# Performance work log

Hardware: AMD Instinct MI355X
Metric: run time of the kernel (lower is better)

## Reference

```python
import jax, jax.numpy as jnp
import numpy as np

B = 32
H = W = 64
C = 128
HEADS = 4
HEAD_DIM = C // HEADS
WS = 8            # window_size
SS = 4            # shift_size
N = WS * WS       # tokens per window
MLP_HID = 4 * C
SCALE = HEAD_DIM ** -0.5
EPS = 1e-5


def _rel_pos_index():
    coords = np.stack(np.meshgrid(np.arange(WS), np.arange(WS), indexing='ij'))
    cf = coords.reshape(2, -1)
    rel = (cf[:, :, None] - cf[:, None, :]).transpose(1, 2, 0)
    rel[:, :, 0] += WS - 1
    rel[:, :, 1] += WS - 1
    rel[:, :, 0] *= 2 * WS - 1
    return rel.sum(-1)  # (N, N) int


def _attn_mask():
    img_mask = np.zeros((1, H, W, 1), np.float32)
    slices = (slice(0, -WS), slice(-WS, -SS), slice(-SS, None))
    cnt = 0
    for hs in slices:
        for ws in slices:
            img_mask[:, hs, ws, :] = cnt
            cnt += 1
    mw = img_mask.reshape(1, H // WS, WS, W // WS, WS, 1)
    mw = mw.transpose(0, 1, 3, 2, 4, 5).reshape(-1, N)  # (nW, N)
    am = mw[:, None, :] - mw[:, :, None]
    return np.where(am != 0, np.float32(-100.0), np.float32(0.0))  # (nW, N, N)


REL_POS_IDX = jnp.asarray(_rel_pos_index().reshape(-1))  # (N*N,)
ATTN_MASK = jnp.asarray(_attn_mask())                    # (nW, N, N)


def setup_inputs() -> dict:
    key = jax.random.key(0)
    ks = jax.random.split(key, 12)
    s = 0.02
    return {
        'x': jax.random.normal(ks[0], (B, H * W, C), jnp.float32),
        'norm1_g': jnp.ones((C,), jnp.float32),
        'norm1_b': jnp.zeros((C,), jnp.float32),
        'qkv_w': jax.random.normal(ks[1], (C, 3 * C), jnp.float32) * s,
        'qkv_b': jnp.zeros((3 * C,), jnp.float32),
        'proj_w': jax.random.normal(ks[2], (C, C), jnp.float32) * s,
        'proj_b': jnp.zeros((C,), jnp.float32),
        'rpb_table': jax.random.normal(ks[3], ((2 * WS - 1) * (2 * WS - 1), HEADS), jnp.float32) * s,
        'norm2_g': jnp.ones((C,), jnp.float32),
        'norm2_b': jnp.zeros((C,), jnp.float32),
        'mlp_w1': jax.random.normal(ks[4], (C, MLP_HID), jnp.float32) * s,
        'mlp_b1': jnp.zeros((MLP_HID,), jnp.float32),
        'mlp_w2': jax.random.normal(ks[5], (MLP_HID, C), jnp.float32) * s,
        'mlp_b2': jnp.zeros((C,), jnp.float32),
    }


def _layernorm(x, g, b):
    m = x.mean(-1, keepdims=True)
    v = jnp.mean((x - m) ** 2, -1, keepdims=True)
    return (x - m) * jax.lax.rsqrt(v + EPS) * g + b


def reference(x, norm1_g, norm1_b, qkv_w, qkv_b, proj_w, proj_b, rpb_table,
              norm2_g, norm2_b, mlp_w1, mlp_b1, mlp_w2, mlp_b2):
    shortcut = x
    h = _layernorm(x, norm1_g, norm1_b).reshape(-1, H, W, C)
    # cyclic shift
    h = jnp.roll(h, (-SS, -SS), axis=(1, 2))
    # window partition -> (B*nW, N, C)
    hw = h.reshape(-1, H // WS, WS, W // WS, WS, C)
    hw = hw.transpose(0, 1, 3, 2, 4, 5).reshape(-1, N, C)
    # window attention
    qkv = (hw @ qkv_w + qkv_b).reshape(-1, N, 3, HEADS, HEAD_DIM)
    qkv = qkv.transpose(2, 0, 3, 1, 4)  # (3, B*nW, heads, N, hd)
    q, k, v = qkv[0] * SCALE, qkv[1], qkv[2]
    attn = jnp.einsum('bhnd,bhmd->bhnm', q, k)  # (B*nW, heads, N, N)
    rpb = rpb_table[REL_POS_IDX].reshape(N, N, HEADS).transpose(2, 0, 1)
    attn = attn + rpb[None]
    nW = ATTN_MASK.shape[0]
    attn = attn.reshape(-1, nW, HEADS, N, N) + ATTN_MASK[None, :, None]
    attn = jax.nn.softmax(attn.reshape(-1, HEADS, N, N), axis=-1)
    out = jnp.einsum('bhnm,bhmd->bhnd', attn, v)
    out = out.transpose(0, 2, 1, 3).reshape(-1, N, C)
    out = out @ proj_w + proj_b
    # window reverse
    out = out.reshape(-1, H // WS, W // WS, WS, WS, C)
    out = out.transpose(0, 1, 3, 2, 4, 5).reshape(-1, H, W, C)
    # reverse cyclic shift
    out = jnp.roll(out, (SS, SS), axis=(1, 2)).reshape(-1, H * W, C)
    x = shortcut + out
    # MLP branch
    h2 = _layernorm(x, norm2_g, norm2_b)
    h2 = jax.nn.gelu(h2 @ mlp_w1 + mlp_b1, approximate=False)
    h2 = h2 @ mlp_w2 + mlp_b2
    return x + h2
```

## Files before the change

### kernel.cpp

```cpp
#include <hip/hip_runtime.h>
#include <math.h>

typedef __attribute__((ext_vector_type(8))) short bf16x8;
typedef __attribute__((ext_vector_type(4))) short bf16x4;
typedef __attribute__((ext_vector_type(4))) float f32x4;
typedef __attribute__((ext_vector_type(4))) unsigned short u16x4;

#define DEVI __device__ __forceinline__

DEVI float b2f(unsigned int u){ union{unsigned int i; float f;} c; c.i = u<<16; return c.f; }
DEVI unsigned short f2b(float f){
  union{float f; unsigned int i;} c; c.f = f;
  unsigned int r = c.i + 0x7fffu + ((c.i>>16)&1u);
  return (unsigned short)(r>>16);
}
DEVI unsigned int pack2(float a, float b){
  return (unsigned int)f2b(a) | ((unsigned int)f2b(b)<<16);
}
DEVI void unpack8(uint4 u, float* f){
  f[0]=b2f(u.x&0xffffu); f[1]=b2f(u.x>>16);
  f[2]=b2f(u.y&0xffffu); f[3]=b2f(u.y>>16);
  f[4]=b2f(u.z&0xffffu); f[5]=b2f(u.z>>16);
  f[6]=b2f(u.w&0xffffu); f[7]=b2f(u.w>>16);
}
DEVI f32x4 mfma16(bf16x8 a, bf16x8 b, f32x4 c){
  return __builtin_amdgcn_mfma_f32_16x16x32_bf16(a, b, c, 0, 0, 0);
}
DEVI f32x4 mfma16x16(bf16x4 a, bf16x4 b, f32x4 c){
#if __has_builtin(__builtin_amdgcn_mfma_f32_16x16x16bf16_1k)
  return __builtin_amdgcn_mfma_f32_16x16x16bf16_1k(a, b, c, 0, 0, 0);
#else
  f32x4 d = c;
  asm volatile("v_mfma_f32_16x16x16_bf16 %0, %1, %2, %0" : "+v"(d) : "v"(a), "v"(b));
  return d;
#endif
}
DEVI float gelu_fast(float u){
  const float y2 = 1.5957691216057308f*(u + 0.044715f*u*u*u);
  return u / (1.f + __expf(-y2));
}
DEVI int swzA(int row, int byi){ return row*256 + (byi ^ ((row&7)<<4)); }
DEVI int swzQ(int row, int byi){ return row*64  + (byi ^ (((row>>1)&3)<<4)); }
DEVI int swzO(int row, int byc){ return row*512 + (byc ^ ((row&7)<<4) ^ (((byc>>7)&3)<<5)); }

__global__ void k_prep(const float* __restrict__ qkvw, const float* __restrict__ projw,
                       const float* __restrict__ w1,   const float* __restrict__ w2,
                       const float* __restrict__ rpbt,
                       ushort* __restrict__ qkvF, ushort* __restrict__ projF,
                       ushort* __restrict__ w1F,  ushort* __restrict__ w2F,
                       ushort* __restrict__ rpbE)
{
  const int t = blockIdx.x*256 + threadIdx.x;
  const int l = t&63, fr = t>>6;
  const int l15 = l&15, l4 = l>>4;
  {
    const int head = t>>12, q = (t>>6)&63, k = t&63;
    const int di = (q>>3)-(k>>3)+7, dj = (q&7)-(k&7)+7;
    rpbE[t] = f2b(rpbt[(di*15+dj)*4 + head]);
  }
  {
    const int c = fr>>5, og = (fr>>2)&7, h = fr&3;
    const int oc = og*16 + l15, hid0 = c*64 + h*16 + l4*4;
    ushort* d = w2F + (size_t)fr*256 + l*4;
    #pragma unroll
    for(int e=0;e<4;e++) d[e] = f2b(w2[(size_t)(hid0+e)*128 + oc]);
  }
  if (fr < 128){
    const int c = fr>>4, hg = (fr>>2)&3, kk = fr&3;
    const int hid = c*64 + hg*16 + l15, k0 = kk*32 + l4*8;
    ushort* d = w1F + (size_t)fr*512 + l*8;
    #pragma unroll
    for(int e=0;e<8;e++) d[e] = f2b(w1[(size_t)(k0+e)*512 + hid]);
  }
  if (fr < 96){
    const int s3 = fr>>5, g = (fr>>2)&7, kk = fr&3;
    const int col = s3*128 + g*16 + l15, k0 = kk*32 + l4*8;
    ushort* d = qkvF + (size_t)fr*512 + l*8;
    #pragma unroll
    for(int e=0;e<8;e++) d[e] = f2b(qkvw[(size_t)(k0+e)*384 + col]);
  }
  if (fr < 32){
    const int g = fr>>2, kk = fr&3;
    const int col = g*16 + l15, k0 = kk*32 + l4*8;
    ushort* d = projF + (size_t)fr*512 + l*8;
    #pragma unroll
    for(int e=0;e<8;e++) d[e] = f2b(projw[(size_t)(k0+e)*128 + col]);
  }
}

__global__ __launch_bounds__(256,3) void k_attn(
    const float*  __restrict__ x,
    const float*  __restrict__ g1, const float* __restrict__ be1,
    const ushort* __restrict__ qkvF, const float* __restrict__ qkvb,
    const ushort* __restrict__ projF, const float* __restrict__ projb,
    const ushort* __restrict__ rpbE,
    ushort* __restrict__ x2w)
{
  __shared__ __align__(16) char smem[49152];
  const int tid  = threadIdx.x;
  const int wave = tid>>6, lane = tid&63;
  const int l15 = lane&15, l4 = lane>>4;
  const int wid = blockIdx.x;
  const int b   = wid>>6, wim = wid&63;
  const int wh  = wim>>3, wv = wim&7;

  char* const smA  = smem;
  char* const smQ  = smem + 16384 + wave*8192;
  char* const smK  = smQ + 4096;
  char* const smR  = smem + 16384;

  const f32x4 Z = {0.f,0.f,0.f,0.f};
  const int t_row = tid>>2;
  const int cg    = (tid&3)*32;
  const int ti_r = t_row>>3, tj_r = t_row&7;
  const int ho_r = (wh*8+ti_r+4)&63, wo_r = (wv*8+tj_r+4)&63;
  const size_t growbase = ((size_t)(b*4096 + ho_r*64 + wo_r))*128;

  {
    const float* src = x + growbase + cg;
    float v[32];
    #pragma unroll
    for(int q=0;q<8;q++){
      const float4 f4 = *(const float4*)(src + q*4);
      v[q*4+0]=f4.x; v[q*4+1]=f4.y; v[q*4+2]=f4.z; v[q*4+3]=f4.w;
    }
    float s=0.f, ss=0.f;
    #pragma unroll
    for(int e=0;e<32;e++){ s+=v[e]; ss+=v[e]*v[e]; }
    s += __shfl_xor(s,1); ss += __shfl_xor(ss,1);
    s += __shfl_xor(s,2); ss += __shfl_xor(ss,2);
    const float mean = s*(1.f/128.f);
    const float varv = fmaxf(ss*(1.f/128.f) - mean*mean, 0.f);
    const float rstd = rsqrtf(varv + 1e-5f);
    #pragma unroll
    for(int q=0;q<4;q++){
      const float4 ga = *(const float4*)(g1 +cg+q*8);
      const float4 gb = *(const float4*)(g1 +cg+q*8+4);
      const float4 ba = *(const float4*)(be1+cg+q*8);
      const float4 bb = *(const float4*)(be1+cg+q*8+4);
      const float* vp = v + q*8;
      uint4 pk;
      pk.x = pack2((vp[0]-mean)*rstd*ga.x+ba.x, (vp[1]-mean)*rstd*ga.y+ba.y);
      pk.y = pack2((vp[2]-mean)*rstd*ga.z+ba.z, (vp[3]-mean)*rstd*ga.w+ba.w);
      pk.z = pack2((vp[4]-mean)*rstd*gb.x+bb.x, (vp[5]-mean)*rstd*gb.y+bb.y);
      pk.w = pack2((vp[6]-mean)*rstd*gb.z+bb.z, (vp[7]-mean)*rstd*gb.w+bb.w);
      *(uint4*)(smA + swzA(t_row, cg*2 + q*16)) = pk;
    }
  }
  __syncthreads();

  const int headc = wave*32;
  bf16x4 Vf[4][2];

  {
    #pragma unroll
    for(int s3=0;s3<3;s3++){
      f32x4 acc[4][2];
      #pragma unroll
      for(int rt=0;rt<4;rt++){ acc[rt][0]=Z; acc[rt][1]=Z; }
      bf16x8 bfr[2][4];
      #pragma unroll
      for(int ct=0;ct<2;ct++)
        #pragma unroll
        for(int kk=0;kk<4;kk++)
          bfr[ct][kk] = *(const bf16x8*)(qkvF + (size_t)((s3*8 + wave*2 + ct)*4 + kk)*512 + lane*8);
      #pragma unroll
      for(int kk=0;kk<4;kk++){
        bf16x8 afr[4];
        #pragma unroll
        for(int rt=0;rt<4;rt++)
          afr[rt] = *(const bf16x8*)(smA + swzA(rt*16+l15, kk*64 + l4*16));
        #pragma unroll
        for(int rt=0;rt<4;rt++)
          #pragma unroll
          for(int ct=0;ct<2;ct++)
            acc[rt][ct] = mfma16(afr[rt], bfr[ct][kk], acc[rt][ct]);
      }
      #pragma unroll
      for(int ct=0;ct<2;ct++){
        const int hd = ct*16 + l15;
        const float bias = qkvb[s3*128 + headc + hd];
        if (s3==2){
          #pragma unroll
          for(int rt=0;rt<4;rt++){
            union { uint2 u; bf16x4 v; } cv;
            cv.u.x = pack2(acc[rt][ct][0]+bias, acc[rt][ct][1]+bias);
            cv.u.y = pack2(acc[rt][ct][2]+bias, acc[rt][ct][3]+bias);
            Vf[rt][ct] = cv.v;
          }
        } else {
          char* const dst = (s3==0) ? smQ : smK;
          const float sc = (s3==0) ? 0.17677669529663687f : 1.f;
          #pragma unroll
          for(int rt=0;rt<4;rt++){
            const int t0 = rt*16 + l4*4;
            #pragma unroll
            for(int j=0;j<4;j++)
              *(ushort*)(dst + swzQ(t0+j, hd*2)) = f2b((acc[rt][ct][j]+bias)*sc);
          }
        }
      }
    }
  }
  __syncthreads();

  f32x4 O[4][2];
  #pragma unroll
  for(int rt=0;rt<4;rt++){ O[rt][0]=Z; O[rt][1]=Z; }
  {
    bf16x8 kfr[4];
    #pragma unroll
    for(int g=0; g<4; ++g)
      kfr[g] = *(const bf16x8*)(smK + swzQ(g*16+l15, l4*16));
    const bool edge = (wh==7) || (wv==7);
    #pragma unroll
    for(int rt=0; rt<4; ++rt){
      const bf16x8 qf = *(const bf16x8*)(smQ + swzQ(rt*16+l15, l4*16));
      f32x4 S[4];
      #pragma unroll
      for(int g=0; g<4; ++g)
        S[g] = mfma16(kfr[g], qf, Z);
      const int q = rt*16 + l15;
      int regq = 0;
      if (edge){
        const int qi=q>>3, qj=q&7;
        regq = ((wh<7)?0:((qi<4)?1:2))*3 + ((wv<7)?0:((qj<4)?1:2));
      }
      const ushort* rbase = rpbE + wave*4096 + q*64 + l4*4;
      #pragma unroll
      for(int g=0; g<4; ++g){
        const u16x4 rb = *(const u16x4*)(rbase + g*16);
        #pragma unroll
        for(int j=0;j<4;j++){
          float add = b2f(rb[j]);
          if (edge){
            const int k = g*16 + l4*4 + j;
            const int ki=k>>3, kj=k&7;
            const int regk = ((wh<7)?0:((ki<4)?1:2))*3 + ((wv<7)?0:((kj<4)?1:2));
            if (regk != regq) add -= 100.f;
          }
          S[g][j] += add;
        }
      }
      float mx = -1e30f;
      #pragma unroll
      for(int g=0;g<4;g++)
        #pragma unroll
        for(int j=0;j<4;j++) mx = fmaxf(mx, S[g][j]);
      mx = fmaxf(mx, __shfl_xor(mx,16));
      mx = fmaxf(mx, __shfl_xor(mx,32));
      float sm = 0.f;
      #pragma unroll
      for(int g=0;g<4;g++)
        #pragma unroll
        for(int j=0;j<4;j++){ const float e = __expf(S[g][j]-mx); S[g][j]=e; sm+=e; }
      sm += __shfl_xor(sm,16);
      sm += __shfl_xor(sm,32);
      const float inv = 1.f/sm;
      #pragma unroll
      for(int g=0;g<4;g++){
        union { uint2 u; bf16x4 v; } cv;
        cv.u.x = pack2(S[g][0]*inv, S[g][1]*inv);
        cv.u.y = pack2(S[g][2]*inv, S[g][3]*inv);
        #pragma unroll
        for(int cvi=0;cvi<2;cvi++)
          O[rt][cvi] = mfma16x16(cv.v, Vf[g][cvi], O[rt][cvi]);
      }
    }
    #pragma unroll
    for(int rt=0;rt<4;rt++)
      #pragma unroll
      for(int cvi=0;cvi<2;cvi++)
        #pragma unroll
        for(int j=0;j<4;j++)
          *(ushort*)(smA + swzA(rt*16+l4*4+j, (headc + cvi*16 + l15)*2)) = f2b(O[rt][cvi][j]);
  }
  __syncthreads();

  {
    f32x4 PR[4][2];
    #pragma unroll
    for(int rt=0;rt<4;rt++){ PR[rt][0]=Z; PR[rt][1]=Z; }
    bf16x8 pb[2][4];
    #pragma unroll
    for(int ct=0;ct<2;ct++)
      #pragma unroll
      for(int kk=0;kk<4;kk++)
        pb[ct][kk] = *(const bf16x8*)(projF + (size_t)((wave*2+ct)*4 + kk)*512 + lane*8);
    #pragma unroll
    for(int kk=0;kk<4;kk++){
      bf16x8 afr[4];
      #pragma unroll
      for(int rt=0;rt<4;rt++)
        afr[rt] = *(const bf16x8*)(smA + swzA(rt*16+l15, kk*64 + l4*16));
      #pragma unroll
      for(int rt=0;rt<4;rt++)
        #pragma unroll
        for(int ct=0;ct<2;ct++)
          PR[rt][ct] = mfma16(afr[rt], pb[ct][kk], PR[rt][ct]);
    }
    #pragma unroll
    for(int ct=0;ct<2;ct++){
      const int col = headc + ct*16 + l15;
      const float bias = projb[col];
      #pragma unroll
      for(int rt=0;rt<4;rt++)
        #pragma unroll
        for(int j=0;j<4;j++)
          *(float*)(smR + swzO(rt*16+l4*4+j, col*4)) = PR[rt][ct][j] + bias;
    }
  }
  __syncthreads();

  {
    const float* xsrc = x + growbase + cg;
    ushort* drow = x2w + ((size_t)(wid*64 + t_row))*128 + cg;
    #pragma unroll
    for(int q=0;q<4;q++){
      const f32x4 oa = *(const f32x4*)(smR + swzO(t_row, (cg+q*8  )*4));
      const f32x4 ob = *(const f32x4*)(smR + swzO(t_row, (cg+q*8+4)*4));
      const float4 xa = *(const float4*)(xsrc + q*8);
      const float4 xb = *(const float4*)(xsrc + q*8+4);
      uint4 pk;
      pk.x = pack2(oa[0]+xa.x, oa[1]+xa.y);
      pk.y = pack2(oa[2]+xa.z, oa[3]+xa.w);
      pk.z = pack2(ob[0]+xb.x, ob[1]+xb.y);
      pk.w = pack2(ob[2]+xb.z, ob[3]+xb.w);
      *(uint4*)(drow + q*8) = pk;
    }
  }
}

__global__ __launch_bounds__(1024) void k_mlp2(
    const ushort* __restrict__ x2w,
    const float* __restrict__ g2, const float* __restrict__ be2,
    const ushort* __restrict__ w1F, const float* __restrict__ bb1,
    const ushort* __restrict__ w2F, const float* __restrict__ bb2,
    float* __restrict__ outp)
{
  __shared__ __align__(16) char smem[65536];
  __shared__ float smB1[512];
  const int tid  = threadIdx.x;
  const int wave = tid>>6, lane = tid&63;
  const int l15 = lane&15, l4 = lane>>4;
  const int gblk = blockIdx.x;
  const f32x4 Z = {0.f,0.f,0.f,0.f};

  if (tid < 512) smB1[tid] = bb1[tid];

  {
    const int tk = tid>>2;
    const int cg = (tid&3)*32;
    const ushort* src = x2w + ((size_t)(gblk*256 + tk))*128 + cg;
    float v[32];
    unpack8(*(const uint4*)(src   ), v   );
    unpack8(*(const uint4*)(src+ 8), v+ 8);
    unpack8(*(const uint4*)(src+16), v+16);
    unpack8(*(const uint4*)(src+24), v+24);
    float s=0.f, ss=0.f;
    #pragma unroll
    for(int e=0;e<32;e++){ s+=v[e]; ss+=v[e]*v[e]; }
    s += __shfl_xor(s,1); ss += __shfl_xor(ss,1);
    s += __shfl_xor(s,2); ss += __shfl_xor(ss,2);
    const float mean = s*(1.f/128.f);
    const float varv = fmaxf(ss*(1.f/128.f) - mean*mean, 0.f);
    const float rstd = rsqrtf(varv + 1e-5f);
    #pragma unroll
    for(int q=0;q<4;q++){
      const float4 ga = *(const float4*)(g2 +cg+q*8);
      const float4 gb = *(const float4*)(g2 +cg+q*8+4);
      const float4 ba = *(const float4*)(be2+cg+q*8);
      const float4 bb = *(const float4*)(be2+cg+q*8+4);
      const float* vp = v + q*8;
      uint4 pk;
      pk.x = pack2((vp[0]-mean)*rstd*ga.x+ba.x, (vp[1]-mean)*rstd*ga.y+ba.y);
      pk.y = pack2((vp[2]-mean)*rstd*ga.z+ba.z, (vp[3]-mean)*rstd*ga.w+ba.w);
      pk.z = pack2((vp[4]-mean)*rstd*gb.x+bb.x, (vp[5]-mean)*rstd*gb.y+bb.y);
      pk.w = pack2((vp[6]-mean)*rstd*gb.z+bb.z, (vp[7]-mean)*rstd*gb.w+bb.w);
      *(uint4*)(smem + swzA(tk, cg*2 + q*16)) = pk;
    }
  }
  __syncthreads();

  const int trow = wave*16 + l15;
  bf16x8 xf[4];
  #pragma unroll
  for(int kk=0;kk<4;++kk)
    xf[kk] = *(const bf16x8*)(smem + swzA(trow, kk*64 + l4*16));
  __syncthreads();

  const ushort* const wsrc = (wave<8) ? w1F : w2F;
  const int ldsoff = ((wave<8)?0:16384) + (wave&7)*2048;
  const int subsh  = (wave&7)*1024;
  #define STAGE_CHUNK(cc, bufbase) do{ \
    const ushort* gsrc = wsrc + (size_t)(cc)*8192 + subsh + lane*8; \
    char* lb = (bufbase) + ldsoff; \
    __builtin_amdgcn_global_load_lds((const unsigned int*)(gsrc     ), (unsigned int*)(lb      ), 16, 0, 0); \
    __builtin_amdgcn_global_load_lds((const unsigned int*)(gsrc+512 ), (unsigned int*)(lb+1024 ), 16, 0, 0); \
  }while(0)

  STAGE_CHUNK(0, smem);
  STAGE_CHUNK(1, smem + 32768);

  f32x4 OA[8];
  #pragma unroll
  for(int ocg=0;ocg<8;++ocg) OA[ocg]=Z;

  for (int c=0; c<8; ++c){
    if (c < 7) asm volatile("s_waitcnt vmcnt(2)" ::: "memory");
    else       asm volatile("s_waitcnt vmcnt(0)" ::: "memory");
    __builtin_amdgcn_s_barrier();
    __builtin_amdgcn_sched_barrier(0);

    char* const buf = (c&1) ? (smem + 32768) : smem;
    const int hidb = c*64;
    f32x4 acc1[4] = {Z,Z,Z,Z};
    #pragma unroll
    for(int hg=0; hg<4; ++hg)
      #pragma unroll
      for(int kk=0; kk<4; ++kk){
        const bf16x8 wf = *(const bf16x8*)(buf + (hg*4+kk)*1024 + lane*16);
        acc1[hg] = mfma16(wf, xf[kk], acc1[hg]);
      }
    bf16x4 Hf[4];
    #pragma unroll
    for(int hg=0; hg<4; ++hg){
      const float4 b4 = *(const float4*)(&smB1[hidb + hg*16 + l4*4]);
      bf16x4 hv;
      hv[0] = (short)f2b(gelu_fast(acc1[hg][0]+b4.x));
      hv[1] = (short)f2b(gelu_fast(acc1[hg][1]+b4.y));
      hv[2] = (short)f2b(gelu_fast(acc1[hg][2]+b4.z));
      hv[3] = (short)f2b(gelu_fast(acc1[hg][3]+b4.w));
      Hf[hg] = hv;
    }
    #pragma unroll
    for(int ocg=0; ocg<8; ++ocg)
      #pragma unroll
      for(int hg=0; hg<4; ++hg){
        const bf16x4 w2f = *(const bf16x4*)(buf + 16384 + (ocg*4+hg)*512 + lane*8);
        OA[ocg] = mfma16x16(w2f, Hf[hg], OA[ocg]);
      }

    __builtin_amdgcn_sched_barrier(0);
    __builtin_amdgcn_s_barrier();
    __builtin_amdgcn_sched_barrier(0);
    if (c < 6) STAGE_CHUNK(c+2, (c&1) ? (smem + 32768) : smem);
  }
  #undef STAGE_CHUNK

  __syncthreads();
  {
    const int tk = tid>>2;
    const int cg = (tid&3)*32;
    const uint4* src = (const uint4*)(x2w + ((size_t)(gblk*256 + tk))*128 + cg);
    #pragma unroll
    for(int q=0;q<4;q++) *(uint4*)(smem + swzA(tk, cg*2 + q*16)) = src[q];
  }
  __syncthreads();
  {
    const int tk  = trow;
    const int wid = gblk*4 + (tk>>6);
    const int n   = tk & 63;
    const int bb  = wid>>6, wim = wid&63;
    const int wh  = wim>>3, wv = wim&7;
    const int ti  = n>>3,  tj = n&7;
    const int ho  = (wh*8+ti+4)&63, wo = (wv*8+tj+4)&63;
    float* const drow = outp + ((size_t)(bb*4096 + ho*64 + wo))*128;
    #pragma unroll
    for(int ocg=0; ocg<8; ++ocg){
      const int oc = ocg*16 + l4*4;
      const float4 b4 = *(const float4*)(bb2 + oc);
      const u16x4 xr = *(const u16x4*)(smem + swzA(tk, oc*2));
      f32x4 r = OA[ocg];
      r[0] += b4.x + b2f(xr[0]);
      r[1] += b4.y + b2f(xr[1]);
      r[2] += b4.z + b2f(xr[2]);
      r[3] += b4.w + b2f(xr[3]);
      __builtin_nontemporal_store(r, (f32x4*)(drow + oc));
    }
  }
}

extern "C" void kernel_launch(void* const* d_in, const int* in_sizes, int n_in,
                              void* d_out, int out_size, void* d_ws, size_t ws_size,
                              hipStream_t stream) {
  (void)in_sizes; (void)n_in; (void)out_size; (void)ws_size;
  const float* x     = (const float*)d_in[0];
  const float* n1g   = (const float*)d_in[1];
  const float* n1b   = (const float*)d_in[2];
  const float* qkvw  = (const float*)d_in[3];
  const float* qkvb  = (const float*)d_in[4];
  const float* projw = (const float*)d_in[5];
  const float* projb = (const float*)d_in[6];
  const float* rpbt  = (const float*)d_in[7];
  const float* n2g   = (const float*)d_in[8];
  const float* n2b   = (const float*)d_in[9];
  const float* w1    = (const float*)d_in[10];
  const float* b1    = (const float*)d_in[11];
  const float* w2    = (const float*)d_in[12];
  const float* b2    = (const float*)d_in[13];
  float* outp = (float*)d_out;

  ushort* ws    = (ushort*)d_ws;
  ushort* x2w   = ws;
  ushort* qkvF  = ws + 16777216;
  ushort* projF = qkvF + 49152;
  ushort* w1F   = projF + 16384;
  ushort* w2F   = w1F + 65536;
  ushort* rpbE  = w2F + 65536;

  k_prep<<<64, 256, 0, stream>>>(qkvw, projw, w1, w2, rpbt, qkvF, projF, w1F, w2F, rpbE);
  k_attn<<<2048, 256, 0, stream>>>(x, n1g, n1b, qkvF, qkvb, projF, projb, rpbE, x2w);
  k_mlp2<<<512, 1024, 0, stream>>>(x2w, n2g, n2b, w1F, b1, w2F, b2, outp);
}
```

Measured before the change: 185.7 us.

## Use hardware bf16 converts, pack W2 fragments, stage MLP output through LDS for coalesced stores

Replaces the software round-to-nearest bf16 packing with the HIP bf16 intrinsics, which may lower to packed convert instructions on this hardware. Reorders the prepared W2 layout so each lane loads 8 bf16 values per LDS read and feeds two 16x16x16 MFMAs, halving the W2 LDS loads. The final MLP output is rounded to bf16 and written to LDS, then re-read row-contiguously so each thread adds residual and bias and writes 32 contiguous floats per row instead of scattered 16-byte pieces. The trade is that the MLP output is now rounded to bf16 before the residual add, which loses precision, and an extra LDS round trip plus barrier is added.

```diff
diff --git a/kernel.cpp b/kernel.cpp
--- a/kernel.cpp
+++ b/kernel.cpp
@@ -1,4 +1,5 @@
 #include <hip/hip_runtime.h>
+#include <hip/hip_bf16.h>
 #include <math.h>
 
 typedef __attribute__((ext_vector_type(8))) short bf16x8;
@@ -14,8 +15,16 @@
   unsigned int r = c.i + 0x7fffu + ((c.i>>16)&1u);
   return (unsigned short)(r>>16);
 }
-DEVI unsigned int pack2(float a, float b){
-  return (unsigned int)f2b(a) | ((unsigned int)f2b(b)<<16);
+DEVI unsigned int cvtpk2(float a, float b){
+  union { __hip_bfloat162 h; unsigned int u; } c;
+  c.h.x = __float2bfloat16(a);
+  c.h.y = __float2bfloat16(b);
+  return c.u;
+}
+DEVI unsigned short f2b1(float a){
+  union { __hip_bfloat16 h; unsigned short u; } c;
+  c.h = __float2bfloat16(a);
+  return c.u;
 }
 DEVI void unpack8(uint4 u, float* f){
   f[0]=b2f(u.x&0xffffu); f[1]=b2f(u.x>>16);
@@ -58,12 +67,16 @@
     const int di = (q>>3)-(k>>3)+7, dj = (q&7)-(k&7)+7;
     rpbE[t] = f2b(rpbt[(di*15+dj)*4 + head]);
   }
-  {
-    const int c = fr>>5, og = (fr>>2)&7, h = fr&3;
-    const int oc = og*16 + l15, hid0 = c*64 + h*16 + l4*4;
-    ushort* d = w2F + (size_t)fr*256 + l*4;
-    #pragma unroll
-    for(int e=0;e<4;e++) d[e] = f2b(w2[(size_t)(hid0+e)*128 + oc]);
+  if (fr < 128){
+    const int c = fr>>4, ocg = (fr>>1)&7, hgp = fr&1;
+    const int oc = ocg*16 + l15;
+    const int hidA = c*64 + (hgp*2)*16 + l4*4;
+    ushort* d = w2F + (size_t)c*8192 + (ocg*2+hgp)*512 + l*8;
+    #pragma unroll
+    for(int e=0;e<4;e++){
+      d[e]   = f2b(w2[(size_t)(hidA+e   )*128 + oc]);
+      d[4+e] = f2b(w2[(size_t)(hidA+16+e)*128 + oc]);
+    }
   }
   if (fr < 128){
     const int c = fr>>4, hg = (fr>>2)&3, kk = fr&3;
@@ -140,10 +153,10 @@
       const float4 bb = *(const float4*)(be1+cg+q*8+4);
       const float* vp = v + q*8;
       uint4 pk;
-      pk.x = pack2((vp[0]-mean)*rstd*ga.x+ba.x, (vp[1]-mean)*rstd*ga.y+ba.y);
-      pk.y = pack2((vp[2]-mean)*rstd*ga.z+ba.z, (vp[3]-mean)*rstd*ga.w+ba.w);
-      pk.z = pack2((vp[4]-mean)*rstd*gb.x+bb.x, (vp[5]-mean)*rstd*gb.y+bb.y);
-      pk.w = pack2((vp[6]-mean)*rstd*gb.z+bb.z, (vp[7]-mean)*rstd*gb.w+bb.w);
+      pk.x = cvtpk2((vp[0]-mean)*rstd*ga.x+ba.x, (vp[1]-mean)*rstd*ga.y+ba.y);
+      pk.y = cvtpk2((vp[2]-mean)*rstd*ga.z+ba.z, (vp[3]-mean)*rstd*ga.w+ba.w);
+      pk.z = cvtpk2((vp[4]-mean)*rstd*gb.x+bb.x, (vp[5]-mean)*rstd*gb.y+bb.y);
+      pk.w = cvtpk2((vp[6]-mean)*rstd*gb.z+bb.z, (vp[7]-mean)*rstd*gb.w+bb.w);
       *(uint4*)(smA + swzA(t_row, cg*2 + q*16)) = pk;
     }
   }
@@ -184,8 +197,8 @@
           #pragma unroll
           for(int rt=0;rt<4;rt++){
             union { uint2 u; bf16x4 v; } cv;
-            cv.u.x = pack2(acc[rt][ct][0]+bias, acc[rt][ct][1]+bias);
-            cv.u.y = pack2(acc[rt][ct][2]+bias, acc[rt][ct][3]+bias);
+            cv.u.x = cvtpk2(acc[rt][ct][0]+bias, acc[rt][ct][1]+bias);
+            cv.u.y = cvtpk2(acc[rt][ct][2]+bias, acc[rt][ct][3]+bias);
             Vf[rt][ct] = cv.v;
           }
         } else {
@@ -196,7 +209,7 @@
             const int t0 = rt*16 + l4*4;
             #pragma unroll
             for(int j=0;j<4;j++)
-              *(ushort*)(dst + swzQ(t0+j, hd*2)) = f2b((acc[rt][ct][j]+bias)*sc);
+              *(ushort*)(dst + swzQ(t0+j, hd*2)) = f2b1((acc[rt][ct][j]+bias)*sc);
           }
         }
       }
@@ -260,8 +273,8 @@
       #pragma unroll
       for(int g=0;g<4;g++){
         union { uint2 u; bf16x4 v; } cv;
-        cv.u.x = pack2(S[g][0]*inv, S[g][1]*inv);
-        cv.u.y = pack2(S[g][2]*inv, S[g][3]*inv);
+        cv.u.x = cvtpk2(S[g][0]*inv, S[g][1]*inv);
+        cv.u.y = cvtpk2(S[g][2]*inv, S[g][3]*inv);
         #pragma unroll
         for(int cvi=0;cvi<2;cvi++)
           O[rt][cvi] = mfma16x16(cv.v, Vf[g][cvi], O[rt][cvi]);
@@ -273,7 +286,7 @@
       for(int cvi=0;cvi<2;cvi++)
         #pragma unroll
         for(int j=0;j<4;j++)
-          *(ushort*)(smA + swzA(rt*16+l4*4+j, (headc + cvi*16 + l15)*2)) = f2b(O[rt][cvi][j]);
+          *(ushort*)(smA + swzA(rt*16+l4*4+j, (headc + cvi*16 + l15)*2)) = f2b1(O[rt][cvi][j]);
   }
   __syncthreads();
 
@@ -322,10 +335,10 @@
       const float4 xa = *(const float4*)(xsrc + q*8);
       const float4 xb = *(const float4*)(xsrc + q*8+4);
       uint4 pk;
-      pk.x = pack2(oa[0]+xa.x, oa[1]+xa.y);
-      pk.y = pack2(oa[2]+xa.z, oa[3]+xa.w);
-      pk.z = pack2(ob[0]+xb.x, ob[1]+xb.y);
-      pk.w = pack2(ob[2]+xb.z, ob[3]+xb.w);
+      pk.x = cvtpk2(oa[0]+xa.x, oa[1]+xa.y);
+      pk.y = cvtpk2(oa[2]+xa.z, oa[3]+xa.w);
+      pk.z = cvtpk2(ob[0]+xb.x, ob[1]+xb.y);
+      pk.w = cvtpk2(ob[2]+xb.z, ob[3]+xb.w);
       *(uint4*)(drow + q*8) = pk;
     }
   }
@@ -373,10 +386,10 @@
       const float4 bb = *(const float4*)(be2+cg+q*8+4);
       const float* vp = v + q*8;
       uint4 pk;
-      pk.x = pack2((vp[0]-mean)*rstd*ga.x+ba.x, (vp[1]-mean)*rstd*ga.y+ba.y);
-      pk.y = pack2((vp[2]-mean)*rstd*ga.z+ba.z, (vp[3]-mean)*rstd*ga.w+ba.w);
-      pk.z = pack2((vp[4]-mean)*rstd*gb.x+bb.x, (vp[5]-mean)*rstd*gb.y+bb.y);
-      pk.w = pack2((vp[6]-mean)*rstd*gb.z+bb.z, (vp[7]-mean)*rstd*gb.w+bb.w);
+      pk.x = cvtpk2((vp[0]-mean)*rstd*ga.x+ba.x, (vp[1]-mean)*rstd*ga.y+ba.y);
+      pk.y = cvtpk2((vp[2]-mean)*rstd*ga.z+ba.z, (vp[3]-mean)*rstd*ga.w+ba.w);
+      pk.z = cvtpk2((vp[4]-mean)*rstd*gb.x+bb.x, (vp[5]-mean)*rstd*gb.y+bb.y);
+      pk.w = cvtpk2((vp[6]-mean)*rstd*gb.z+bb.z, (vp[7]-mean)*rstd*gb.w+bb.w);
       *(uint4*)(smem + swzA(tk, cg*2 + q*16)) = pk;
     }
   }
@@ -426,19 +439,20 @@
     #pragma unroll
     for(int hg=0; hg<4; ++hg){
       const float4 b4 = *(const float4*)(&smB1[hidb + hg*16 + l4*4]);
-      bf16x4 hv;
-      hv[0] = (short)f2b(gelu_fast(acc1[hg][0]+b4.x));
-      hv[1] = (short)f2b(gelu_fast(acc1[hg][1]+b4.y));
-      hv[2] = (short)f2b(gelu_fast(acc1[hg][2]+b4.z));
-      hv[3] = (short)f2b(gelu_fast(acc1[hg][3]+b4.w));
-      Hf[hg] = hv;
+      union { uint2 u; bf16x4 v; } cv;
+      cv.u.x = cvtpk2(gelu_fast(acc1[hg][0]+b4.x), gelu_fast(acc1[hg][1]+b4.y));
+      cv.u.y = cvtpk2(gelu_fast(acc1[hg][2]+b4.z), gelu_fast(acc1[hg][3]+b4.w));
+      Hf[hg] = cv.v;
     }
     #pragma unroll
     for(int ocg=0; ocg<8; ++ocg)
       #pragma unroll
-      for(int hg=0; hg<4; ++hg){
-        const bf16x4 w2f = *(const bf16x4*)(buf + 16384 + (ocg*4+hg)*512 + lane*8);
-        OA[ocg] = mfma16x16(w2f, Hf[hg], OA[ocg]);
+      for(int hgp=0; hgp<2; ++hgp){
+        const bf16x8 wp = *(const bf16x8*)(buf + 16384 + (ocg*2+hgp)*1024 + lane*16);
+        const bf16x4 wlo = __builtin_shufflevector(wp, wp, 0,1,2,3);
+        const bf16x4 whi = __builtin_shufflevector(wp, wp, 4,5,6,7);
+        OA[ocg] = mfma16x16(wlo, Hf[hgp*2  ], OA[ocg]);
+        OA[ocg] = mfma16x16(whi, Hf[hgp*2+1], OA[ocg]);
       }
 
     __builtin_amdgcn_sched_barrier(0);
@@ -450,33 +464,44 @@
 
   __syncthreads();
   {
+    #pragma unroll
+    for(int ocg=0; ocg<8; ++ocg){
+      const int oc = ocg*16 + l4*4;
+      uint2 pk;
+      pk.x = cvtpk2(OA[ocg][0], OA[ocg][1]);
+      pk.y = cvtpk2(OA[ocg][2], OA[ocg][3]);
+      *(uint2*)(smem + swzA(trow, oc*2)) = pk;
+    }
+  }
+  __syncthreads();
+  {
     const int tk = tid>>2;
     const int cg = (tid&3)*32;
-    const uint4* src = (const uint4*)(x2w + ((size_t)(gblk*256 + tk))*128 + cg);
-    #pragma unroll
-    for(int q=0;q<4;q++) *(uint4*)(smem + swzA(tk, cg*2 + q*16)) = src[q];
-  }
-  __syncthreads();
-  {
-    const int tk  = trow;
     const int wid = gblk*4 + (tk>>6);
     const int n   = tk & 63;
     const int bb  = wid>>6, wim = wid&63;
     const int wh  = wim>>3, wv = wim&7;
     const int ti  = n>>3,  tj = n&7;
     const int ho  = (wh*8+ti+4)&63, wo = (wv*8+tj+4)&63;
-    float* const drow = outp + ((size_t)(bb*4096 + ho*64 + wo))*128;
-    #pragma unroll
-    for(int ocg=0; ocg<8; ++ocg){
-      const int oc = ocg*16 + l4*4;
-      const float4 b4 = *(const float4*)(bb2 + oc);
-      const u16x4 xr = *(const u16x4*)(smem + swzA(tk, oc*2));
-      f32x4 r = OA[ocg];
-      r[0] += b4.x + b2f(xr[0]);
-      r[1] += b4.y + b2f(xr[1]);
-      r[2] += b4.z + b2f(xr[2]);
-      r[3] += b4.w + b2f(xr[3]);
-      __builtin_nontemporal_store(r, (f32x4*)(drow + oc));
+    float* const drow = outp + ((size_t)(bb*4096 + ho*64 + wo))*128 + cg;
+    const ushort* x2src = x2w + ((size_t)(gblk*256 + tk))*128 + cg;
+    #pragma unroll
+    for(int q=0;q<4;q++){
+      const uint4 oa = *(const uint4*)(smem + swzA(tk, cg*2 + q*16));
+      const uint4 xr = *(const uint4*)(x2src + q*8);
+      const float4 ba = *(const float4*)(bb2 + cg + q*8);
+      const float4 bbv= *(const float4*)(bb2 + cg + q*8 + 4);
+      f32x4 r0, r1;
+      r0[0] = b2f(oa.x&0xffffu)+b2f(xr.x&0xffffu)+ba.x;
+      r0[1] = b2f(oa.x>>16    )+b2f(xr.x>>16    )+ba.y;
+      r0[2] = b2f(oa.y&0xffffu)+b2f(xr.y&0xffffu)+ba.z;
+      r0[3] = b2f(oa.y>>16    )+b2f(xr.y>>16    )+ba.w;
+      r1[0] = b2f(oa.z&0xffffu)+b2f(xr.z&0xffffu)+bbv.x;
+      r1[1] = b2f(oa.z>>16    )+b2f(xr.z>>16    )+bbv.y;
+      r1[2] = b2f(oa.w&0xffffu)+b2f(xr.w&0xffffu)+bbv.z;
+      r1[3] = b2f(oa.w>>16    )+b2f(xr.w>>16    )+bbv.w;
+      __builtin_nontemporal_store(r0, (f32x4*)(drow + q*8));
+      __builtin_nontemporal_store(r1, (f32x4*)(drow + q*8 + 4));
     }
   }
 }
```

Result: slower. 263.1 us (+41.7%).
